# Kernel optimization log

Measured on AMD Instinct MI355X. Metric: run time of the kernel, lower is better.

Reference implementation:

```python
import jax, jax.numpy as jnp
import numpy as np

EMBED_DIM = 1024
NUM_HEADS = 16
HEAD_DIM = EMBED_DIM // NUM_HEADS
R = 8
ALPHA = 32
SCALING = ALPHA / R


def setup_inputs() -> dict:
    key = jax.random.key(0)
    ks = jax.random.split(key, 12)
    d = EMBED_DIM
    s = 1.0 / np.sqrt(d)
    inp = {
        "x": jax.random.normal(ks[0], (4, 2048, d), dtype=jnp.float32),
        # base linear weights (torch layout: [out, in]) and biases
        "Wq": jax.random.normal(ks[1], (d, d), dtype=jnp.float32) * s,
        "bq": jax.random.normal(ks[2], (d,), dtype=jnp.float32) * s,
        "Wk": jax.random.normal(ks[3], (d, d), dtype=jnp.float32) * s,
        "bk": jax.random.normal(ks[4], (d,), dtype=jnp.float32) * s,
        "Wv": jax.random.normal(ks[5], (d, d), dtype=jnp.float32) * s,
        "bv": jax.random.normal(ks[6], (d,), dtype=jnp.float32) * s,
        "Wo": jax.random.normal(ks[7], (d, d), dtype=jnp.float32) * s,
        "bo": jax.random.normal(ks[8], (d,), dtype=jnp.float32) * s,
        # LoRA adapters for q and v: A [r, in], B [out, r]
        "Aq": jax.random.normal(ks[9], (R, d), dtype=jnp.float32) * s,
        "Bq": jnp.zeros((d, R), dtype=jnp.float32),
        "Av": jax.random.normal(ks[10], (R, d), dtype=jnp.float32) * s,
        "Bv": jnp.zeros((d, R), dtype=jnp.float32),
    }
    return inp


def _lora_linear(x, W, b, A, Bm):
    # base: x @ W.T + b ; lora: scaling * (x @ A.T) @ B.T
    return x @ W.T + b + SCALING * ((x @ A.T) @ Bm.T)


def reference(x, Wq, bq, Wk, bk, Wv, bv, Wo, bo, Aq, Bq, Av, Bv):
    B, T, C = x.shape
    H, D = NUM_HEADS, HEAD_DIM
    q = _lora_linear(x, Wq, bq, Aq, Bq)
    k = x @ Wk.T + bk
    v = _lora_linear(x, Wv, bv, Av, Bv)
    # [B, T, C] -> [B, H, T, D]
    q = q.reshape(B, T, H, D).transpose(0, 2, 1, 3)
    k = k.reshape(B, T, H, D).transpose(0, 2, 1, 3)
    v = v.reshape(B, T, H, D).transpose(0, 2, 1, 3)
    scores = jnp.einsum("bhqd,bhkd->bhqk", q, k) / np.sqrt(D).astype(np.float32)
    weights = jax.nn.softmax(scores, axis=-1)
    out = jnp.einsum("bhqk,bhkd->bhqd", weights, v)
    out = out.transpose(0, 2, 1, 3).reshape(B, T, C)
    return out @ Wo.T + bo
```

## Files before the change

### kernel.cpp

```cpp
#include <hip/hip_runtime.h>
#include <hip/hip_bf16.h>
#include <stdint.h>

namespace {
constexpr int kB = 4, kT = 2048, kC = 1024, kH = 16, kD = 64;
constexpr int kM = kB * kT;
constexpr int kR = 8;
constexpr float kScaling = 4.0f;
constexpr float kQScale = 0.125f * 1.4426950408889634f;
}

typedef short short8 __attribute__((ext_vector_type(8)));
typedef float f32x4 __attribute__((ext_vector_type(4)));
typedef unsigned short ushort4v __attribute__((ext_vector_type(4)));
typedef unsigned short ushort8v __attribute__((ext_vector_type(8)));
typedef unsigned int uint2v __attribute__((ext_vector_type(2)));

__device__ inline unsigned short bf16_bits(float f) {
  __hip_bfloat16 h = __float2bfloat16(f);
  unsigned short u;
  __builtin_memcpy(&u, &h, 2);
  return u;
}
__device__ inline float bits_f(unsigned short u) {
  return __uint_as_float((uint32_t)u << 16);
}
__device__ inline void split1(float f, unsigned short& h, unsigned short& l) {
  h = bf16_bits(f);
  l = bf16_bits(f - bits_f(h));
}
__device__ inline uint32_t cvtpk2(float a, float b) {
  __hip_bfloat162 h2 = __float22bfloat162_rn(float2{a, b});
  uint32_t u;
  __builtin_memcpy(&u, &h2, 4);
  return u;
}

__global__ __launch_bounds__(256) void pack_kernel(
    const float* __restrict__ s, unsigned short* __restrict__ hp,
    unsigned short* __restrict__ lp, int n4) {
  int i = blockIdx.x * 256 + threadIdx.x;
  const int stride = gridDim.x * 256;
  for (; i < n4; i += stride) {
    const float4 v = reinterpret_cast<const float4*>(s)[i];
    const float f[4] = {v.x, v.y, v.z, v.w};
    ushort4v h, l;
#pragma unroll
    for (int j = 0; j < 4; ++j) {
      unsigned short hb, lb;
      split1(f[j], hb, lb);
      h[j] = hb;
      l[j] = lb;
    }
    reinterpret_cast<ushort4v*>(hp)[i] = h;
    reinterpret_cast<ushort4v*>(lp)[i] = l;
  }
}

__global__ __launch_bounds__(256) void lora_xa_kernel(
    const float* __restrict__ x, const float* __restrict__ Aq,
    const float* __restrict__ Av, float* __restrict__ xa) {
  const int wave = threadIdx.x >> 6;
  const int lane = threadIdx.x & 63;
  const int row = (blockIdx.x << 2) + wave;
  const float4* xr = reinterpret_cast<const float4*>(x) + (size_t)row * (kC / 4);
  const float4* aq = reinterpret_cast<const float4*>(Aq);
  const float4* av = reinterpret_cast<const float4*>(Av);
  float acc[16];
#pragma unroll
  for (int r = 0; r < 16; ++r) acc[r] = 0.f;
#pragma unroll
  for (int jj = 0; jj < (kC / 4) / 64; ++jj) {
    const int j = lane + jj * 64;
    const float4 xv = xr[j];
#pragma unroll
    for (int r = 0; r < 8; ++r) {
      const float4 a = aq[r * (kC / 4) + j];
      acc[r] += xv.x * a.x + xv.y * a.y + xv.z * a.z + xv.w * a.w;
      const float4 b = av[r * (kC / 4) + j];
      acc[8 + r] += xv.x * b.x + xv.y * b.y + xv.z * b.z + xv.w * b.w;
    }
  }
#pragma unroll
  for (int r = 0; r < 16; ++r) {
    float v = acc[r];
#pragma unroll
    for (int off = 32; off > 0; off >>= 1) v += __shfl_xor(v, off, 64);
    if (lane == 0) xa[(size_t)row * 16 + r] = v;
  }
}

__global__ __launch_bounds__(256, 2) void gemm_planes_kernel(
    const unsigned short* __restrict__ Ah_g, const unsigned short* __restrict__ Al_g,
    const unsigned short* __restrict__ Bh_g, const unsigned short* __restrict__ Bl_g,
    const float* __restrict__ bias, const float* __restrict__ xa,
    const float* __restrict__ Bm,
    unsigned short* __restrict__ o16a, unsigned short* __restrict__ o16b,
    float* __restrict__ o32,
    const int lora_sel, const int out_mode, const float out_scale) {
  constexpr int BK = 32;
  __shared__ __align__(16) unsigned char sA[128 * 128];
  __shared__ __align__(16) unsigned char sB[128 * 128];

  const int tid = threadIdx.x;
  const int m0 = blockIdx.y << 7;
  const int n0 = blockIdx.x << 7;
  const int wave = tid >> 6, lane = tid & 63;
  const int wr = wave >> 1, wc = wave & 1;
  const int lrow = lane & 15;
  const int lkg = lane >> 4;

  const int srow = tid >> 1;
  const int sc0 = (tid & 1) << 1;
  const unsigned short* pa_h = Ah_g + (size_t)(m0 + srow) * kC + sc0 * 8;
  const unsigned short* pa_l = Al_g + (size_t)(m0 + srow) * kC + sc0 * 8;
  const unsigned short* pb_h = Bh_g + (size_t)(n0 + srow) * kC + sc0 * 8;
  const unsigned short* pb_l = Bl_g + (size_t)(n0 + srow) * kC + sc0 * 8;

  f32x4 acc[4][4];
#pragma unroll
  for (int a = 0; a < 4; ++a)
#pragma unroll
    for (int b = 0; b < 4; ++b) acc[a][b] = (f32x4){0.f, 0.f, 0.f, 0.f};

  ushort8v rah[2], ral[2], rbh[2], rbl[2];
#pragma unroll
  for (int j = 0; j < 2; ++j) {
    rah[j] = *reinterpret_cast<const ushort8v*>(pa_h + j * 8);
    ral[j] = *reinterpret_cast<const ushort8v*>(pa_l + j * 8);
    rbh[j] = *reinterpret_cast<const ushort8v*>(pb_h + j * 8);
    rbl[j] = *reinterpret_cast<const ushort8v*>(pb_l + j * 8);
  }

  for (int k0 = 0; k0 < kC; k0 += BK) {
    const int rbase = srow * 128;
    const int s7 = srow & 7;
#pragma unroll
    for (int j = 0; j < 2; ++j) {
      const int c = sc0 + j;
      *reinterpret_cast<ushort8v*>(&sA[rbase + ((c ^ s7) << 4)]) = rah[j];
      *reinterpret_cast<ushort8v*>(&sA[rbase + (((c | 4) ^ s7) << 4)]) = ral[j];
      *reinterpret_cast<ushort8v*>(&sB[rbase + ((c ^ s7) << 4)]) = rbh[j];
      *reinterpret_cast<ushort8v*>(&sB[rbase + (((c | 4) ^ s7) << 4)]) = rbl[j];
    }
    __syncthreads();

    if (k0 + BK < kC) {
      const int kn = k0 + BK;
#pragma unroll
      for (int j = 0; j < 2; ++j) {
        rah[j] = *reinterpret_cast<const ushort8v*>(pa_h + kn + j * 8);
        ral[j] = *reinterpret_cast<const ushort8v*>(pa_l + kn + j * 8);
        rbh[j] = *reinterpret_cast<const ushort8v*>(pb_h + kn + j * 8);
        rbl[j] = *reinterpret_cast<const ushort8v*>(pb_l + kn + j * 8);
      }
    }

    short8 ah[4], al[4];
#pragma unroll
    for (int rb = 0; rb < 4; ++rb) {
      const int rA = wr * 64 + rb * 16 + lrow;
      ah[rb] = *reinterpret_cast<const short8*>(&sA[rA * 128 + ((lkg ^ (rA & 7)) << 4)]);
      al[rb] = *reinterpret_cast<const short8*>(&sA[rA * 128 + (((lkg | 4) ^ (rA & 7)) << 4)]);
    }
#pragma unroll
    for (int cb = 0; cb < 4; ++cb) {
      const int rB = wc * 64 + cb * 16 + lrow;
      const short8 bhf = *reinterpret_cast<const short8*>(&sB[rB * 128 + ((lkg ^ (rB & 7)) << 4)]);
      const short8 blf = *reinterpret_cast<const short8*>(&sB[rB * 128 + (((lkg | 4) ^ (rB & 7)) << 4)]);
#pragma unroll
      for (int rb = 0; rb < 4; ++rb) {
        acc[rb][cb] = __builtin_amdgcn_mfma_f32_16x16x32_bf16(ah[rb], bhf, acc[rb][cb], 0, 0, 0);
        acc[rb][cb] = __builtin_amdgcn_mfma_f32_16x16x32_bf16(ah[rb], blf, acc[rb][cb], 0, 0, 0);
        acc[rb][cb] = __builtin_amdgcn_mfma_f32_16x16x32_bf16(al[rb], bhf, acc[rb][cb], 0, 0, 0);
      }
    }
    __syncthreads();
  }

#pragma unroll
  for (int rb = 0; rb < 4; ++rb) {
    const int mbase = m0 + wr * 64 + rb * 16 + (lkg << 2);
    float la2[4][kR];
    if (lora_sel >= 0) {
#pragma unroll
      for (int i = 0; i < 4; ++i)
#pragma unroll
        for (int r = 0; r < kR; ++r)
          la2[i][r] = xa[(size_t)(mbase + i) * 16 + lora_sel + r];
    }
#pragma unroll
    for (int cb = 0; cb < 4; ++cb) {
      const int n = n0 + wc * 64 + cb * 16 + lrow;
      const float bi = bias[n];
      float vv[4];
#pragma unroll
      for (int i = 0; i < 4; ++i) {
        vv[i] = acc[rb][cb][i] + bi;
        if (lora_sel >= 0) {
          float lv = 0.f;
#pragma unroll
          for (int r = 0; r < kR; ++r)
            lv = fmaf(la2[i][r], Bm[(size_t)n * kR + r], lv);
          vv[i] += kScaling * lv;
        }
        vv[i] *= out_scale;
      }
      if (out_mode == 1) {
        const int bb_ = mbase >> 11;
        const int t0 = mbase & (kT - 1);
        const int hh = n >> 6;
        const int dd = n & (kD - 1);
#pragma unroll
        for (int i = 0; i < 4; ++i) {
          const size_t off = (((size_t)bb_ * kH + hh) * kT + t0 + i) * kD + dd;
          unsigned short hb, lb;
          split1(vv[i], hb, lb);
          o16a[off] = hb;
          o16b[off] = lb;
        }
      } else if (out_mode == 2) {
        const int bb_ = mbase >> 11;
        const int t0 = mbase & (kT - 1);
        const int hh = n >> 6;
        const int dd = n & (kD - 1);
        ushort4v w;
#pragma unroll
        for (int i = 0; i < 4; ++i) w[i] = bf16_bits(vv[i]);
        *reinterpret_cast<ushort4v*>(
            o16a + (((size_t)bb_ * kH + hh) * kD + dd) * kT + t0) = w;
      } else {
#pragma unroll
        for (int i = 0; i < 4; ++i)
          o32[(size_t)(mbase + i) * kC + n] = vv[i];
      }
    }
  }
}

__global__ __launch_bounds__(256) void attn_mfma_kernel(
    const unsigned short* __restrict__ Qh, const unsigned short* __restrict__ Ql,
    const unsigned short* __restrict__ Kh_g, const unsigned short* __restrict__ Kl_g,
    const unsigned short* __restrict__ Vt_g,
    unsigned short* __restrict__ ctx_h, unsigned short* __restrict__ ctx_l) {
  __shared__ __align__(16) unsigned char sKh[64 * 128];
  __shared__ __align__(16) unsigned char sKl[64 * 128];
  __shared__ __align__(16) unsigned char sVt[64 * 128];
  __shared__ __align__(16) unsigned char sP[128 * 128];

  const int tid = threadIdx.x;
  const int wave = tid >> 6, lane = tid & 63;
  const int lrow = lane & 15, lg = lane >> 4;
  const int bh = blockIdx.y;
  const int q0 = blockIdx.x << 7;
  const int b = bh >> 4, h = bh & 15;

  short8 qh[2][2], ql[2][2];
#pragma unroll
  for (int qs = 0; qs < 2; ++qs)
#pragma unroll
    for (int d0 = 0; d0 < 2; ++d0) {
      const size_t off =
          ((size_t)bh * kT + q0 + wave * 32 + qs * 16 + lrow) * kD + d0 * 32 + lg * 8;
      qh[qs][d0] = *reinterpret_cast<const short8*>(Qh + off);
      ql[qs][d0] = *reinterpret_cast<const short8*>(Ql + off);
    }

  const int srow = tid >> 2;
  const int sc0 = (tid & 3) << 1;
  const unsigned short* khs = Kh_g + ((size_t)bh * kT + srow) * kD + sc0 * 8;
  const unsigned short* kls = Kl_g + ((size_t)bh * kT + srow) * kD + sc0 * 8;
  const unsigned short* vts = Vt_g + ((size_t)bh * kD + srow) * kT + sc0 * 8;

  f32x4 acc_o[2][4];
#pragma unroll
  for (int qs = 0; qs < 2; ++qs)
#pragma unroll
    for (int dr = 0; dr < 4; ++dr) acc_o[qs][dr] = (f32x4){0.f, 0.f, 0.f, 0.f};
  float m_i[2] = {-3.0e38f, -3.0e38f};
  float l_i[2] = {0.f, 0.f};

  constexpr int kNT = kT / 64;
  ushort8v kph[2], kpl[2], vpv[2];
#pragma unroll
  for (int j = 0; j < 2; ++j) {
    kph[j] = *reinterpret_cast<const ushort8v*>(khs + j * 8);
    kpl[j] = *reinterpret_cast<const ushort8v*>(kls + j * 8);
    vpv[j] = *reinterpret_cast<const ushort8v*>(vts + j * 8);
  }

  for (int kt = 0; kt < kNT; ++kt) {
    {
      const int rb2 = srow * 128;
      const int s7 = srow & 7;
#pragma unroll
      for (int j = 0; j < 2; ++j) {
        const int c = sc0 + j;
        *reinterpret_cast<ushort8v*>(&sKh[rb2 + ((c ^ s7) << 4)]) = kph[j];
        *reinterpret_cast<ushort8v*>(&sKl[rb2 + ((c ^ s7) << 4)]) = kpl[j];
        *reinterpret_cast<ushort8v*>(&sVt[rb2 + ((c ^ s7) << 4)]) = vpv[j];
      }
    }
    __syncthreads();

    if (kt + 1 < kNT) {
      const size_t koffK = (size_t)(kt + 1) * 64 * kD;
      const int koffV = (kt + 1) * 64;
#pragma unroll
      for (int j = 0; j < 2; ++j) {
        kph[j] = *reinterpret_cast<const ushort8v*>(khs + koffK + j * 8);
        kpl[j] = *reinterpret_cast<const ushort8v*>(kls + koffK + j * 8);
        vpv[j] = *reinterpret_cast<const ushort8v*>(vts + koffV + j * 8);
      }
    }

    f32x4 acc_s[2][4];
#pragma unroll
    for (int qs = 0; qs < 2; ++qs)
#pragma unroll
      for (int kvr = 0; kvr < 4; ++kvr) acc_s[qs][kvr] = (f32x4){0.f, 0.f, 0.f, 0.f};
#pragma unroll
    for (int d0 = 0; d0 < 2; ++d0) {
#pragma unroll
      for (int kvr = 0; kvr < 4; ++kvr) {
        const int rk = kvr * 16 + lrow;
        const int byt = rk * 128 + ((((d0 << 2) + lg) ^ (rk & 7)) << 4);
        const short8 khf = *reinterpret_cast<const short8*>(&sKh[byt]);
        const short8 klf = *reinterpret_cast<const short8*>(&sKl[byt]);
#pragma unroll
        for (int qs = 0; qs < 2; ++qs) {
          acc_s[qs][kvr] = __builtin_amdgcn_mfma_f32_16x16x32_bf16(khf, qh[qs][d0], acc_s[qs][kvr], 0, 0, 0);
          acc_s[qs][kvr] = __builtin_amdgcn_mfma_f32_16x16x32_bf16(khf, ql[qs][d0], acc_s[qs][kvr], 0, 0, 0);
          acc_s[qs][kvr] = __builtin_amdgcn_mfma_f32_16x16x32_bf16(klf, qh[qs][d0], acc_s[qs][kvr], 0, 0, 0);
        }
      }
    }

#pragma unroll
    for (int qs = 0; qs < 2; ++qs) {
      float mx = acc_s[qs][0][0];
#pragma unroll
      for (int kvr = 0; kvr < 4; ++kvr)
#pragma unroll
        for (int i = 0; i < 4; ++i) mx = fmaxf(mx, acc_s[qs][kvr][i]);
      mx = fmaxf(mx, __shfl_xor(mx, 16, 64));
      mx = fmaxf(mx, __shfl_xor(mx, 32, 64));
      const float mnew = fmaxf(m_i[qs], mx);
      const float alpha = __builtin_exp2f(m_i[qs] - mnew);
      m_i[qs] = mnew;
      const int prow = wave * 32 + qs * 16 + lrow;
      const int p7 = prow & 7;
      float rs = 0.f;
#pragma unroll
      for (int kvr = 0; kvr < 4; ++kvr) {
        float p[4];
#pragma unroll
        for (int i = 0; i < 4; ++i) {
          p[i] = __builtin_exp2f(acc_s[qs][kvr][i] - mnew);
          rs += p[i];
        }
        uint2v pu;
        pu[0] = cvtpk2(p[0], p[1]);
        pu[1] = cvtpk2(p[2], p[3]);
        const int chunk = ((kvr << 1) + (lg >> 1)) ^ p7;
        *reinterpret_cast<uint2v*>(&sP[prow * 128 + (chunk << 4) + ((lg & 1) << 3)]) = pu;
      }
      rs += __shfl_xor(rs, 16, 64);
      rs += __shfl_xor(rs, 32, 64);
      l_i[qs] = l_i[qs] * alpha + rs;
#pragma unroll
      for (int dr = 0; dr < 4; ++dr)
#pragma unroll
        for (int i = 0; i < 4; ++i) acc_o[qs][dr][i] *= alpha;
    }
    __builtin_amdgcn_sched_barrier(0);

#pragma unroll
    for (int ks = 0; ks < 2; ++ks) {
      short8 pf[2];
#pragma unroll
      for (int qs = 0; qs < 2; ++qs) {
        const int prow = wave * 32 + qs * 16 + lrow;
        pf[qs] = *reinterpret_cast<const short8*>(
            &sP[prow * 128 + ((((ks << 2) + lg) ^ (prow & 7)) << 4)]);
      }
#pragma unroll
      for (int dr = 0; dr < 4; ++dr) {
        const int rv = dr * 16 + lrow;
        const short8 vf = *reinterpret_cast<const short8*>(
            &sVt[rv * 128 + ((((ks << 2) + lg) ^ (rv & 7)) << 4)]);
        acc_o[0][dr] = __builtin_amdgcn_mfma_f32_16x16x32_bf16(vf, pf[0], acc_o[0][dr], 0, 0, 0);
        acc_o[1][dr] = __builtin_amdgcn_mfma_f32_16x16x32_bf16(vf, pf[1], acc_o[1][dr], 0, 0, 0);
      }
    }
    __syncthreads();
  }

#pragma unroll
  for (int qs = 0; qs < 2; ++qs) {
    const float inv = 1.0f / l_i[qs];
    const int qq = q0 + wave * 32 + qs * 16 + lrow;
    const size_t base = ((size_t)b * kT + qq) * kC + (h << 6);
#pragma unroll
    for (int dr = 0; dr < 4; ++dr) {
      ushort4v wh, wl;
#pragma unroll
      for (int i = 0; i < 4; ++i) {
        unsigned short hb, lb;
        split1(acc_o[qs][dr][i] * inv, hb, lb);
        wh[i] = hb;
        wl[i] = lb;
      }
      *reinterpret_cast<ushort4v*>(ctx_h + base + dr * 16 + (lg << 2)) = wh;
      *reinterpret_cast<ushort4v*>(ctx_l + base + dr * 16 + (lg << 2)) = wl;
    }
  }
}

extern "C" void kernel_launch(void* const* d_in, const int* in_sizes, int n_in,
                              void* d_out, int out_size, void* d_ws, size_t ws_size,
                              hipStream_t stream) {
  const float* x  = (const float*)d_in[0];
  const float* Wq = (const float*)d_in[1];
  const float* bq = (const float*)d_in[2];
  const float* Wk = (const float*)d_in[3];
  const float* bk = (const float*)d_in[4];
  const float* Wv = (const float*)d_in[5];
  const float* bv = (const float*)d_in[6];
  const float* Wo = (const float*)d_in[7];
  const float* bo = (const float*)d_in[8];
  const float* Aq = (const float*)d_in[9];
  const float* Bq = (const float*)d_in[10];
  const float* Av = (const float*)d_in[11];
  const float* Bv = (const float*)d_in[12];
  float* out = (float*)d_out;

  constexpr size_t MP = (size_t)kM * kC;
  constexpr size_t WP = (size_t)kC * kC;
  unsigned short* w16 = (unsigned short*)d_ws;
  unsigned short* Xh  = w16;
  unsigned short* Xl  = Xh  + MP;
  unsigned short* Wqh = Xl  + MP;
  unsigned short* Wql = Wqh + WP;
  unsigned short* Wkh = Wql + WP;
  unsigned short* Wkl = Wkh + WP;
  unsigned short* Wvh = Wkl + WP;
  unsigned short* Wvl = Wvh + WP;
  unsigned short* Woh = Wvl + WP;
  unsigned short* Wol = Woh + WP;
  unsigned short* Qh  = Wol + WP;
  unsigned short* Ql  = Qh  + MP;
  unsigned short* Kh  = Ql  + MP;
  unsigned short* Kl  = Kh  + MP;
  unsigned short* Vt  = Kl  + MP;
  float* xa = (float*)(Vt + MP);

  hipLaunchKernelGGL(pack_kernel, dim3(2048), dim3(256), 0, stream, x, Xh, Xl, (int)(MP / 4));
  hipLaunchKernelGGL(pack_kernel, dim3(1024), dim3(256), 0, stream, Wq, Wqh, Wql, (int)(WP / 4));
  hipLaunchKernelGGL(pack_kernel, dim3(1024), dim3(256), 0, stream, Wk, Wkh, Wkl, (int)(WP / 4));
  hipLaunchKernelGGL(pack_kernel, dim3(1024), dim3(256), 0, stream, Wv, Wvh, Wvl, (int)(WP / 4));
  hipLaunchKernelGGL(pack_kernel, dim3(1024), dim3(256), 0, stream, Wo, Woh, Wol, (int)(WP / 4));

  hipLaunchKernelGGL(lora_xa_kernel, dim3(kM / 4), dim3(256), 0, stream, x, Aq, Av, xa);

  const dim3 gg(kC / 128, kM / 128);
  hipLaunchKernelGGL(gemm_planes_kernel, gg, dim3(256), 0, stream,
                     Xh, Xl, Wqh, Wql, bq, xa, Bq, Qh, Ql, nullptr, 0, 1, kQScale);
  hipLaunchKernelGGL(gemm_planes_kernel, gg, dim3(256), 0, stream,
                     Xh, Xl, Wkh, Wkl, bk, nullptr, nullptr, Kh, Kl, nullptr, -1, 1, 1.0f);
  hipLaunchKernelGGL(gemm_planes_kernel, gg, dim3(256), 0, stream,
                     Xh, Xl, Wvh, Wvl, bv, xa, Bv, Vt, nullptr, nullptr, 8, 2, 1.0f);

  hipLaunchKernelGGL(attn_mfma_kernel, dim3(kT / 128, kB * kH), dim3(256), 0, stream,
                     Qh, Ql, Kh, Kl, Vt, Xh, Xl);

  hipLaunchKernelGGL(gemm_planes_kernel, gg, dim3(256), 0, stream,
                     Xh, Xl, Woh, Wol, bo, nullptr, nullptr, nullptr, nullptr, out, -1, 0, 1.0f);
}
```

Before: 710.5 us.

## Load GEMM and attention tiles straight to LDS with global_load_lds

```diff
diff --git a/kernel.cpp b/kernel.cpp
--- a/kernel.cpp
+++ b/kernel.cpp
@@ -13,7 +13,6 @@
 typedef short short8 __attribute__((ext_vector_type(8)));
 typedef float f32x4 __attribute__((ext_vector_type(4)));
 typedef unsigned short ushort4v __attribute__((ext_vector_type(4)));
-typedef unsigned short ushort8v __attribute__((ext_vector_type(8)));
 typedef unsigned int uint2v __attribute__((ext_vector_type(2)));
 
 __device__ inline unsigned short bf16_bits(float f) {
@@ -34,6 +33,11 @@
   uint32_t u;
   __builtin_memcpy(&u, &h2, 4);
   return u;
+}
+__device__ inline void gload_lds16(const void* g, void* l) {
+  __builtin_amdgcn_global_load_lds(
+      (const __attribute__((address_space(1))) unsigned int*)g,
+      (__attribute__((address_space(3))) unsigned int*)l, 16, 0, 0);
 }
 
 __global__ __launch_bounds__(256) void pack_kernel(
@@ -90,7 +94,7 @@
   }
 }
 
-__global__ __launch_bounds__(256, 2) void gemm_planes_kernel(
+__global__ __launch_bounds__(256, 4) void gemm_planes_kernel(
     const unsigned short* __restrict__ Ah_g, const unsigned short* __restrict__ Al_g,
     const unsigned short* __restrict__ Bh_g, const unsigned short* __restrict__ Bl_g,
     const float* __restrict__ bias, const float* __restrict__ xa,
@@ -110,12 +114,17 @@
   const int lrow = lane & 15;
   const int lkg = lane >> 4;
 
-  const int srow = tid >> 1;
-  const int sc0 = (tid & 1) << 1;
-  const unsigned short* pa_h = Ah_g + (size_t)(m0 + srow) * kC + sc0 * 8;
-  const unsigned short* pa_l = Al_g + (size_t)(m0 + srow) * kC + sc0 * 8;
-  const unsigned short* pb_h = Bh_g + (size_t)(n0 + srow) * kC + sc0 * 8;
-  const unsigned short* pb_l = Bl_g + (size_t)(n0 + srow) * kC + sc0 * 8;
+  const int seg_r = lane >> 3;
+  const int cs = (lane & 7) ^ seg_r;
+  const int cc8 = (cs & 3) * 8;
+  const unsigned short* srcA[4];
+  const unsigned short* srcB[4];
+#pragma unroll
+  for (int i = 0; i < 4; ++i) {
+    const int r = wave * 32 + i * 8 + seg_r;
+    srcA[i] = (cs < 4 ? Ah_g : Al_g) + (size_t)(m0 + r) * kC + cc8;
+    srcB[i] = (cs < 4 ? Bh_g : Bl_g) + (size_t)(n0 + r) * kC + cc8;
+  }
 
   f32x4 acc[4][4];
 #pragma unroll
@@ -123,38 +132,13 @@
 #pragma unroll
     for (int b = 0; b < 4; ++b) acc[a][b] = (f32x4){0.f, 0.f, 0.f, 0.f};
 
-  ushort8v rah[2], ral[2], rbh[2], rbl[2];
-#pragma unroll
-  for (int j = 0; j < 2; ++j) {
-    rah[j] = *reinterpret_cast<const ushort8v*>(pa_h + j * 8);
-    ral[j] = *reinterpret_cast<const ushort8v*>(pa_l + j * 8);
-    rbh[j] = *reinterpret_cast<const ushort8v*>(pb_h + j * 8);
-    rbl[j] = *reinterpret_cast<const ushort8v*>(pb_l + j * 8);
-  }
-
   for (int k0 = 0; k0 < kC; k0 += BK) {
-    const int rbase = srow * 128;
-    const int s7 = srow & 7;
-#pragma unroll
-    for (int j = 0; j < 2; ++j) {
-      const int c = sc0 + j;
-      *reinterpret_cast<ushort8v*>(&sA[rbase + ((c ^ s7) << 4)]) = rah[j];
-      *reinterpret_cast<ushort8v*>(&sA[rbase + (((c | 4) ^ s7) << 4)]) = ral[j];
-      *reinterpret_cast<ushort8v*>(&sB[rbase + ((c ^ s7) << 4)]) = rbh[j];
-      *reinterpret_cast<ushort8v*>(&sB[rbase + (((c | 4) ^ s7) << 4)]) = rbl[j];
+#pragma unroll
+    for (int i = 0; i < 4; ++i) {
+      gload_lds16(srcA[i] + k0, &sA[wave * 4096 + i * 1024]);
+      gload_lds16(srcB[i] + k0, &sB[wave * 4096 + i * 1024]);
     }
     __syncthreads();
-
-    if (k0 + BK < kC) {
-      const int kn = k0 + BK;
-#pragma unroll
-      for (int j = 0; j < 2; ++j) {
-        rah[j] = *reinterpret_cast<const ushort8v*>(pa_h + kn + j * 8);
-        ral[j] = *reinterpret_cast<const ushort8v*>(pa_l + kn + j * 8);
-        rbh[j] = *reinterpret_cast<const ushort8v*>(pb_h + kn + j * 8);
-        rbl[j] = *reinterpret_cast<const ushort8v*>(pb_l + kn + j * 8);
-      }
-    }
 
     short8 ah[4], al[4];
 #pragma unroll
@@ -238,7 +222,7 @@
   }
 }
 
-__global__ __launch_bounds__(256) void attn_mfma_kernel(
+__global__ __launch_bounds__(256, 4) void attn_mfma_kernel(
     const unsigned short* __restrict__ Qh, const unsigned short* __restrict__ Ql,
     const unsigned short* __restrict__ Kh_g, const unsigned short* __restrict__ Kl_g,
     const unsigned short* __restrict__ Vt_g,
@@ -266,11 +250,18 @@
       ql[qs][d0] = *reinterpret_cast<const short8*>(Ql + off);
     }
 
-  const int srow = tid >> 2;
-  const int sc0 = (tid & 3) << 1;
-  const unsigned short* khs = Kh_g + ((size_t)bh * kT + srow) * kD + sc0 * 8;
-  const unsigned short* kls = Kl_g + ((size_t)bh * kT + srow) * kD + sc0 * 8;
-  const unsigned short* vts = Vt_g + ((size_t)bh * kD + srow) * kT + sc0 * 8;
+  const int seg_r = lane >> 3;
+  const int cs8 = ((lane & 7) ^ seg_r) * 8;
+  const unsigned short* srcKh[2];
+  const unsigned short* srcKl[2];
+  const unsigned short* srcVt[2];
+#pragma unroll
+  for (int i = 0; i < 2; ++i) {
+    const int r = wave * 16 + i * 8 + seg_r;
+    srcKh[i] = Kh_g + ((size_t)bh * kT + r) * kD + cs8;
+    srcKl[i] = Kl_g + ((size_t)bh * kT + r) * kD + cs8;
+    srcVt[i] = Vt_g + ((size_t)bh * kD + r) * kT + cs8;
+  }
 
   f32x4 acc_o[2][4];
 #pragma unroll
@@ -281,38 +272,16 @@
   float l_i[2] = {0.f, 0.f};
 
   constexpr int kNT = kT / 64;
-  ushort8v kph[2], kpl[2], vpv[2];
-#pragma unroll
-  for (int j = 0; j < 2; ++j) {
-    kph[j] = *reinterpret_cast<const ushort8v*>(khs + j * 8);
-    kpl[j] = *reinterpret_cast<const ushort8v*>(kls + j * 8);
-    vpv[j] = *reinterpret_cast<const ushort8v*>(vts + j * 8);
-  }
-
   for (int kt = 0; kt < kNT; ++kt) {
-    {
-      const int rb2 = srow * 128;
-      const int s7 = srow & 7;
-#pragma unroll
-      for (int j = 0; j < 2; ++j) {
-        const int c = sc0 + j;
-        *reinterpret_cast<ushort8v*>(&sKh[rb2 + ((c ^ s7) << 4)]) = kph[j];
-        *reinterpret_cast<ushort8v*>(&sKl[rb2 + ((c ^ s7) << 4)]) = kpl[j];
-        *reinterpret_cast<ushort8v*>(&sVt[rb2 + ((c ^ s7) << 4)]) = vpv[j];
-      }
+    const size_t koffK = (size_t)kt * 64 * kD;
+    const int koffV = kt * 64;
+#pragma unroll
+    for (int i = 0; i < 2; ++i) {
+      gload_lds16(srcKh[i] + koffK, &sKh[wave * 2048 + i * 1024]);
+      gload_lds16(srcKl[i] + koffK, &sKl[wave * 2048 + i * 1024]);
+      gload_lds16(srcVt[i] + koffV, &sVt[wave * 2048 + i * 1024]);
     }
     __syncthreads();
-
-    if (kt + 1 < kNT) {
-      const size_t koffK = (size_t)(kt + 1) * 64 * kD;
-      const int koffV = (kt + 1) * 64;
-#pragma unroll
-      for (int j = 0; j < 2; ++j) {
-        kph[j] = *reinterpret_cast<const ushort8v*>(khs + koffK + j * 8);
-        kpl[j] = *reinterpret_cast<const ushort8v*>(kls + koffK + j * 8);
-        vpv[j] = *reinterpret_cast<const ushort8v*>(vts + koffV + j * 8);
-      }
-    }
 
     f32x4 acc_s[2][4];
 #pragma unroll
```

Result: slower. 826.6 us (+16.4%).
